# Kernel optimization log

Hardware: AMD Instinct MI355X
Metric: run time of the kernel (lower is better)

Reference implementation:

```python
import jax, jax.numpy as jnp
import numpy as np

N, D, H, E, K = 8192, 1024, 4096, 8, 2


def setup_inputs() -> dict:
    key = jax.random.key(0)
    ks = jax.random.split(key, 4)
    scaled = lambda k, shp, fan: (jax.random.normal(k, shp, jnp.float32) / np.sqrt(fan).astype(np.float32))
    return {
        "x": jax.random.normal(ks[0], (N, D), jnp.float32),
        "Wg": scaled(ks[1], (D, E), D),
        "bg": jnp.zeros((E,), jnp.float32),
        "W1": scaled(ks[2], (E, D, H), D),
        "b1": jnp.zeros((E, H), jnp.float32),
        "W2": scaled(ks[3], (E, H, D), H),
        "b2": jnp.zeros((E, D), jnp.float32),
    }


def reference(x, Wg, bg, W1, b1, W2, b2):
    # Gating: softmax over experts, top-k selection, renormalize top-k probs.
    gate_probs = jax.nn.softmax(x @ Wg + bg, axis=-1)            # [N, E]
    topk_p, topk_i = jax.lax.top_k(gate_probs, K)                # [N, K]
    topk_p = topk_p / topk_p.sum(axis=-1, keepdims=True)
    onehot = jax.nn.one_hot(topk_i, E, dtype=x.dtype)            # [N, K, E]
    # Per-token combine weight for each expert (0 if expert not in top-k).
    w = (onehot * topk_p[..., None]).sum(axis=1)                 # [N, E]

    out = jnp.zeros_like(x)
    for e in range(E):  # fixed small loop over structurally distinct experts
        h = jax.nn.relu(x @ W1[e] + b1[e])                       # dropout = identity (eval)
        out = out + w[:, e:e + 1] * (h @ W2[e] + b2[e])

    # Load-balancing auxiliary loss.
    importance = gate_probs.sum(axis=0)
    importance = importance / importance.sum()
    load = onehot.sum(axis=(0, 1)) / (x.shape[0] * K)            # [E]
    lb_loss = E * (importance * load).sum()
    return out, lb_loss
```

## Files before the change

kernel.cpp:

```cpp
#include <hip/hip_runtime.h>
#include <hip/hip_bf16.h>
#include <math.h>

#define NTOK 8192
#define DDIM 1024
#define HDIM 4096
#define NEXP 8
#define KTOP 2
#define MAXROWS 17408
#define MAXTILES 136

typedef __bf16 bf16x8 __attribute__((ext_vector_type(8)));
typedef float f32x4 __attribute__((ext_vector_type(4)));

#define GAS __attribute__((address_space(1)))
#define LAS __attribute__((address_space(3)))

__device__ __forceinline__ void async16(const void* g, void* l) {
  __builtin_amdgcn_global_load_lds((GAS void*)g, (LAS void*)l, 16, 0, 0);
}

#define XB_OFF     ((size_t)0)
#define W1T_OFF    (XB_OFF + (size_t)NTOK*DDIM*2)
#define ROWOUT_OFF W1T_OFF
#define W2T_OFF    (W1T_OFF + (size_t)NEXP*DDIM*HDIM*2)
#define HB_OFF     (W2T_OFF + (size_t)NEXP*HDIM*DDIM*2)
#define ROWTOK_OFF (HB_OFF + (size_t)MAXROWS*HDIM*2)
#define ROWW_OFF   (ROWTOK_OFF + (size_t)MAXROWS*4)
#define TOKE_OFF   (ROWW_OFF + (size_t)MAXROWS*4)
#define TOKW_OFF   (TOKE_OFF + (size_t)NTOK*KTOP*4)
#define TOKROW_OFF (TOKW_OFF + (size_t)NTOK*KTOP*4)
#define TILEE_OFF  (TOKROW_OFF + (size_t)NTOK*KTOP*4)
#define CNT_OFF    (TILEE_OFF + (size_t)256*4)
#define POS_OFF    (CNT_OFF + 64)
#define IMP_OFF    (POS_OFF + 64)
#define META_OFF   (IMP_OFF + 64)

__global__ void init_kernel(int* counts, float* importance) {
  if (threadIdx.x < NEXP) { counts[threadIdx.x] = 0; importance[threadIdx.x] = 0.f; }
}

__global__ void cast_x_kernel(const float* __restrict__ src, __hip_bfloat16* __restrict__ dst) {
  size_t i = ((size_t)blockIdx.x * blockDim.x + threadIdx.x) * 4;
  if (i < (size_t)NTOK * DDIM) {
    float4 v = *(const float4*)(src + i);
    dst[i + 0] = __float2bfloat16(v.x);
    dst[i + 1] = __float2bfloat16(v.y);
    dst[i + 2] = __float2bfloat16(v.z);
    dst[i + 3] = __float2bfloat16(v.w);
  }
}

__global__ __launch_bounds__(256) void transpose_cast_kernel(
    const float* __restrict__ src, __hip_bfloat16* __restrict__ dst, int R, int C) {
  __shared__ float tile[64][65];
  const int e = blockIdx.z;
  const float* s = src + (size_t)e * R * C;
  __hip_bfloat16* d = dst + (size_t)e * R * C;
  const int c0 = blockIdx.x * 64, r0 = blockIdx.y * 64;
  const int tc = (threadIdx.x & 15) * 4;
  const int tr = threadIdx.x >> 4;
#pragma unroll
  for (int p = 0; p < 4; ++p) {
    float4 v = *(const float4*)&s[(size_t)(r0 + tr + p * 16) * C + c0 + tc];
    tile[tr + p * 16][tc + 0] = v.x;
    tile[tr + p * 16][tc + 1] = v.y;
    tile[tr + p * 16][tc + 2] = v.z;
    tile[tr + p * 16][tc + 3] = v.w;
  }
  __syncthreads();
  const int oc = threadIdx.x >> 4;
  const int orr = (threadIdx.x & 15) * 4;
#pragma unroll
  for (int p = 0; p < 4; ++p) {
    const int c = oc + p * 16;
    __hip_bfloat16 tmp[4];
    tmp[0] = __float2bfloat16(tile[orr + 0][c]);
    tmp[1] = __float2bfloat16(tile[orr + 1][c]);
    tmp[2] = __float2bfloat16(tile[orr + 2][c]);
    tmp[3] = __float2bfloat16(tile[orr + 3][c]);
    *(ushort4*)&d[(size_t)(c0 + c) * R + r0 + orr] = *(ushort4*)tmp;
  }
}

__global__ __launch_bounds__(256) void gating_kernel(
    const float* __restrict__ x, const float* __restrict__ Wg, const float* __restrict__ bg,
    int* __restrict__ tok_e, float* __restrict__ tok_w,
    int* __restrict__ counts, float* __restrict__ importance) {
  const int tid = threadIdx.x, wid = tid >> 6, lane = tid & 63;
  const int t = blockIdx.x * 32 + wid * 8 + (lane >> 3);
  const int e = lane & 7;
  const float* xr = x + (size_t)t * DDIM;
  double dot = 0.0;
  for (int d = 0; d < DDIM; d += 4) {
    float4 xv = *(const float4*)(xr + d);
    dot += (double)xv.x * (double)Wg[(d + 0) * NEXP + e];
    dot += (double)xv.y * (double)Wg[(d + 1) * NEXP + e];
    dot += (double)xv.z * (double)Wg[(d + 2) * NEXP + e];
    dot += (double)xv.w * (double)Wg[(d + 3) * NEXP + e];
  }
  double logit = dot + (double)bg[e];
  double m = logit;
  for (int off = 1; off < 8; off <<= 1) {
    double o = __shfl_xor(m, off, 64);
    m = o > m ? o : m;
  }
  double p = exp(logit - m);
  double s = p;
  for (int off = 1; off < 8; off <<= 1) s += __shfl_xor(s, off, 64);
  float prob = (float)(p / s);

  __shared__ float imp[NEXP];
  __shared__ int cnt[NEXP];
  if (tid < NEXP) { imp[tid] = 0.f; cnt[tid] = 0; }
  __syncthreads();
  atomicAdd(&imp[e], prob);

  float bp = prob; int be = e;
  for (int off = 1; off < 8; off <<= 1) {
    float op = __shfl_xor(bp, off, 64); int oe = __shfl_xor(be, off, 64);
    if (op > bp || (op == bp && oe < be)) { bp = op; be = oe; }
  }
  float p2 = (e == be) ? -1.f : prob;
  float sp = p2; int se = e;
  for (int off = 1; off < 8; off <<= 1) {
    float op = __shfl_xor(sp, off, 64); int oe = __shfl_xor(se, off, 64);
    if (op > sp || (op == sp && oe < se)) { sp = op; se = oe; }
  }
  if (e == 0) {
    float tsum = bp + sp;
    tok_e[t * 2 + 0] = be; tok_e[t * 2 + 1] = se;
    tok_w[t * 2 + 0] = bp / tsum; tok_w[t * 2 + 1] = sp / tsum;
    atomicAdd(&cnt[be], 1); atomicAdd(&cnt[se], 1);
  }
  __syncthreads();
  if (tid < NEXP) {
    atomicAdd(&counts[tid], cnt[tid]);
    atomicAdd(&importance[tid], imp[tid]);
  }
}

__global__ void offsets_kernel(const int* __restrict__ counts, int* pos, int* tile_expert,
                               int* meta, int* row_token) {
  if (threadIdx.x == 0) {
    int pb = 0, tb = 0;
    for (int e = 0; e < NEXP; e++) {
      pos[e] = pb;
      int tiles = (counts[e] + 127) >> 7;
      for (int tt = 0; tt < tiles; ++tt) tile_expert[tb + tt] = e;
      pb += tiles * 128; tb += tiles;
    }
    meta[0] = tb;
  }
  __syncthreads();
  for (int i = threadIdx.x; i < MAXROWS; i += blockDim.x) row_token[i] = -1;
}

__global__ void scatter_kernel(const int* __restrict__ tok_e, const float* __restrict__ tok_w,
                               int* __restrict__ pos, int* __restrict__ row_token,
                               float* __restrict__ row_weight, int* __restrict__ tok_row) {
  __shared__ int lcnt[NEXP], lbase[NEXP];
  const int t = blockIdx.x * 256 + threadIdx.x;
  if (threadIdx.x < NEXP) lcnt[threadIdx.x] = 0;
  __syncthreads();
  const int e0 = tok_e[t * 2 + 0], e1 = tok_e[t * 2 + 1];
  const int s0 = atomicAdd(&lcnt[e0], 1);
  const int s1 = atomicAdd(&lcnt[e1], 1);
  __syncthreads();
  if (threadIdx.x < NEXP) lbase[threadIdx.x] = atomicAdd(&pos[threadIdx.x], lcnt[threadIdx.x]);
  __syncthreads();
  int r0 = lbase[e0] + s0; row_token[r0] = t; row_weight[r0] = tok_w[t * 2 + 0]; tok_row[t * 2 + 0] = r0;
  int r1 = lbase[e1] + s1; row_token[r1] = t; row_weight[r1] = tok_w[t * 2 + 1]; tok_row[t * 2 + 1] = r1;
}

template<int NDIM, int KDIM, int NCOLT, bool GATHER, bool RELU>
__global__ __launch_bounds__(512, 2) void moe_gemm_kernel(
    const __hip_bfloat16* __restrict__ Ag, const __hip_bfloat16* __restrict__ Bg,
    const float* __restrict__ bias, __hip_bfloat16* __restrict__ Cg,
    const int* __restrict__ row_token, const int* __restrict__ tile_expert,
    const int* __restrict__ meta) {
  const int id = blockIdx.x;
  const int v = (id & 7) * ((int)gridDim.x >> 3) + (id >> 3);
  const int ty = v / NCOLT, cx = v % NCOLT;
  if (ty >= meta[0]) return;
  const int e = tile_expert[ty];
  const int r0 = ty * 128;
  const int n0 = cx * 256;
  const int tid = threadIdx.x, wid = tid >> 6, lane = tid & 63;
  const int wm = wid >> 2, wn = wid & 3;
  const int fr = lane & 15;
  const int NT = KDIM / 64;

  __shared__ __align__(16) __hip_bfloat16 Al[2][128][64];
  __shared__ __align__(16) __hip_bfloat16 Bl[2][256][64];

  const int l8 = lane >> 3;
  const int gsrc = (lane & 7) ^ l8;
  const __hip_bfloat16* aptr[2];
  const __hip_bfloat16* bptr0[2];
  const __hip_bfloat16* bptr1[2];
#pragma unroll
  for (int i = 0; i < 2; ++i) {
    const int c = wid * 2 + i;
    const int arow = r0 + c * 8 + l8;
    if (GATHER) {
      int t = row_token[arow]; if (t < 0) t = 0;
      aptr[i] = Ag + (size_t)t * KDIM + gsrc * 8;
    } else {
      aptr[i] = Ag + (size_t)arow * KDIM + gsrc * 8;
    }
    bptr0[i] = Bg + ((size_t)e * NDIM + n0 + c * 8 + l8) * KDIM + gsrc * 8;
    bptr1[i] = bptr0[i] + (size_t)128 * KDIM;
  }

#define ST_A(buf, kk)  do { _Pragma("unroll") for (int i = 0; i < 2; ++i) \
    async16(aptr[i]  + (kk) * 64, &Al[buf][(wid * 2 + i) * 8][0]); } while (0)
#define ST_B0(buf, kk) do { _Pragma("unroll") for (int i = 0; i < 2; ++i) \
    async16(bptr0[i] + (kk) * 64, &Bl[buf][(wid * 2 + i) * 8][0]); } while (0)
#define ST_B1(buf, kk) do { _Pragma("unroll") for (int i = 0; i < 2; ++i) \
    async16(bptr1[i] + (kk) * 64, &Bl[buf][128 + (wid * 2 + i) * 8][0]); } while (0)

  const int g4 = lane >> 4, r7 = lane & 7;
  const int s0e = ((0 + g4) ^ r7) * 8;
  const int s1e = ((4 + g4) ^ r7) * 8;

  f32x4 acc[4][4] = {};

  ST_A(0, 0); ST_B0(0, 0); ST_B1(0, 0);
  ST_A(1, 1); ST_B0(1, 1);
  asm volatile("s_waitcnt vmcnt(6)" ::: "memory");
  __builtin_amdgcn_sched_barrier(0);
  __builtin_amdgcn_s_barrier();

#pragma unroll 1
  for (int kt = 0; kt < NT; ++kt) {
    const int cur = kt & 1, nxt = cur ^ 1;
    const int kk1 = (kt + 1 < NT) ? kt + 1 : NT - 1;
    const int kk2 = (kt + 2 < NT) ? kt + 2 : NT - 1;
    bf16x8 av[4][2], bv[2][2];
#pragma unroll
    for (int mi = 0; mi < 4; ++mi) {
      av[mi][0] = *(const bf16x8*)&Al[cur][wm * 64 + mi * 16 + fr][s0e];
      av[mi][1] = *(const bf16x8*)&Al[cur][wm * 64 + mi * 16 + fr][s1e];
    }
#pragma unroll
    for (int j = 0; j < 2; ++j) {
      bv[j][0] = *(const bf16x8*)&Bl[cur][wn * 32 + j * 16 + fr][s0e];
      bv[j][1] = *(const bf16x8*)&Bl[cur][wn * 32 + j * 16 + fr][s1e];
    }
    ST_B1(nxt, kk1);
    __builtin_amdgcn_s_barrier();
    asm volatile("s_waitcnt lgkmcnt(0)" ::: "memory");
    __builtin_amdgcn_sched_barrier(0);
    __builtin_amdgcn_s_setprio(1);
#pragma unroll
    for (int mi = 0; mi < 4; ++mi)
#pragma unroll
      for (int j = 0; j < 2; ++j)
#pragma unroll
        for (int k = 0; k < 2; ++k)
          acc[mi][j] = __builtin_amdgcn_mfma_f32_16x16x32_bf16(av[mi][k], bv[j][k], acc[mi][j], 0, 0, 0);
    __builtin_amdgcn_s_setprio(0);
    asm volatile("s_waitcnt vmcnt(6)" ::: "memory");
    __builtin_amdgcn_sched_barrier(0);
    __builtin_amdgcn_s_barrier();
#pragma unroll
    for (int j = 0; j < 2; ++j) {
      bv[j][0] = *(const bf16x8*)&Bl[cur][128 + wn * 32 + j * 16 + fr][s0e];
      bv[j][1] = *(const bf16x8*)&Bl[cur][128 + wn * 32 + j * 16 + fr][s1e];
    }
    ST_A(cur, kk2); ST_B0(cur, kk2);
    __builtin_amdgcn_s_barrier();
    asm volatile("s_waitcnt lgkmcnt(0)" ::: "memory");
    __builtin_amdgcn_sched_barrier(0);
    __builtin_amdgcn_s_setprio(1);
#pragma unroll
    for (int mi = 0; mi < 4; ++mi)
#pragma unroll
      for (int j = 0; j < 2; ++j)
#pragma unroll
        for (int k = 0; k < 2; ++k)
          acc[mi][2 + j] = __builtin_amdgcn_mfma_f32_16x16x32_bf16(av[mi][k], bv[j][k], acc[mi][2 + j], 0, 0, 0);
    __builtin_amdgcn_s_setprio(0);
    asm volatile("s_waitcnt vmcnt(6)" ::: "memory");
    __builtin_amdgcn_sched_barrier(0);
    __builtin_amdgcn_s_barrier();
  }
#undef ST_A
#undef ST_B0
#undef ST_B1
  asm volatile("s_waitcnt vmcnt(0)" ::: "memory");

  const int crow = (lane >> 4) * 4;
  const int ccol = lane & 15;
#pragma unroll
  for (int nj = 0; nj < 4; ++nj) {
    const int gc = n0 + (nj >> 1) * 128 + wn * 32 + (nj & 1) * 16 + ccol;
    const float bv_ = bias[e * NDIM + gc];
#pragma unroll
    for (int mi = 0; mi < 4; ++mi) {
      const int grb = r0 + wm * 64 + mi * 16 + crow;
#pragma unroll
      for (int r = 0; r < 4; ++r) {
        float vv = acc[mi][nj][r] + bv_;
        if (RELU) vv = vv > 0.f ? vv : 0.f;
        Cg[(size_t)(grb + r) * NDIM + gc] = __float2bfloat16(vv);
      }
    }
  }
}

__global__ __launch_bounds__(256) void combine_kernel(
    const __hip_bfloat16* __restrict__ rowout, const int* __restrict__ tok_row,
    const float* __restrict__ row_weight, float* __restrict__ out) {
  const int idx = blockIdx.x * 256 + threadIdx.x;
  const int t = idx >> 7;
  const int d = (idx & 127) * 8;
  const int r0 = tok_row[t * 2 + 0], r1 = tok_row[t * 2 + 1];
  const float w0 = row_weight[r0], w1 = row_weight[r1];
  bf16x8 a = *(const bf16x8*)&rowout[(size_t)r0 * DDIM + d];
  bf16x8 b = *(const bf16x8*)&rowout[(size_t)r1 * DDIM + d];
  float o[8];
#pragma unroll
  for (int k = 0; k < 8; k++) o[k] = w0 * (float)a[k] + w1 * (float)b[k];
  float* dst = out + (size_t)t * DDIM + d;
  *(float4*)(dst + 0) = make_float4(o[0], o[1], o[2], o[3]);
  *(float4*)(dst + 4) = make_float4(o[4], o[5], o[6], o[7]);
}

__global__ void finalize_kernel(const float* __restrict__ importance,
                                const int* __restrict__ counts, float* __restrict__ lb_out) {
  if (threadIdx.x == 0 && blockIdx.x == 0) {
    float s = 0.f;
    for (int e = 0; e < NEXP; e++) s += importance[e];
    float lb = 0.f;
    for (int e = 0; e < NEXP; e++)
      lb += (importance[e] / s) * ((float)counts[e] / (float)(NTOK * KTOP));
    lb_out[0] = (float)NEXP * lb;
  }
}

extern "C" void kernel_launch(void* const* d_in, const int* in_sizes, int n_in,
                              void* d_out, int out_size, void* d_ws, size_t ws_size,
                              hipStream_t stream) {
  (void)in_sizes; (void)n_in; (void)out_size; (void)ws_size;
  const float* x  = (const float*)d_in[0];
  const float* Wg = (const float*)d_in[1];
  const float* bg = (const float*)d_in[2];
  const float* W1 = (const float*)d_in[3];
  const float* b1 = (const float*)d_in[4];
  const float* W2 = (const float*)d_in[5];
  const float* b2 = (const float*)d_in[6];
  float* out = (float*)d_out;

  char* ws = (char*)d_ws;
  __hip_bfloat16* xb     = (__hip_bfloat16*)(ws + XB_OFF);
  __hip_bfloat16* w1t    = (__hip_bfloat16*)(ws + W1T_OFF);
  __hip_bfloat16* rowout = (__hip_bfloat16*)(ws + ROWOUT_OFF);
  __hip_bfloat16* w2t    = (__hip_bfloat16*)(ws + W2T_OFF);
  __hip_bfloat16* hb     = (__hip_bfloat16*)(ws + HB_OFF);
  int*   row_token  = (int*)(ws + ROWTOK_OFF);
  float* row_weight = (float*)(ws + ROWW_OFF);
  int*   tok_e   = (int*)(ws + TOKE_OFF);
  float* tok_w   = (float*)(ws + TOKW_OFF);
  int*   tok_row = (int*)(ws + TOKROW_OFF);
  int*   tile_e  = (int*)(ws + TILEE_OFF);
  int*   counts  = (int*)(ws + CNT_OFF);
  int*   pos     = (int*)(ws + POS_OFF);
  float* importance = (float*)(ws + IMP_OFF);
  int*   meta    = (int*)(ws + META_OFF);

  init_kernel<<<1, 64, 0, stream>>>(counts, importance);
  cast_x_kernel<<<NTOK * DDIM / 4 / 256, 256, 0, stream>>>(x, xb);
  transpose_cast_kernel<<<dim3(HDIM / 64, DDIM / 64, NEXP), 256, 0, stream>>>(W1, w1t, DDIM, HDIM);
  transpose_cast_kernel<<<dim3(DDIM / 64, HDIM / 64, NEXP), 256, 0, stream>>>(W2, w2t, HDIM, DDIM);
  gating_kernel<<<NTOK / 32, 256, 0, stream>>>(x, Wg, bg, tok_e, tok_w, counts, importance);
  offsets_kernel<<<1, 256, 0, stream>>>(counts, pos, tile_e, meta, row_token);
  scatter_kernel<<<NTOK / 256, 256, 0, stream>>>(tok_e, tok_w, pos, row_token, row_weight, tok_row);
  moe_gemm_kernel<HDIM, DDIM, HDIM / 256, true, true>
      <<<MAXTILES * (HDIM / 256), 512, 0, stream>>>(xb, w1t, b1, hb, row_token, tile_e, meta);
  moe_gemm_kernel<DDIM, HDIM, DDIM / 256, false, false>
      <<<MAXTILES * (DDIM / 256), 512, 0, stream>>>(hb, w2t, b2, rowout, row_token, tile_e, meta);
  combine_kernel<<<NTOK * 128 / 256, 256, 0, stream>>>(rowout, tok_row, row_weight, out);
  finalize_kernel<<<1, 64, 0, stream>>>(importance, counts, out + (size_t)NTOK * DDIM);
}
```

Before: 839.1 us.

## Enlarge MoE GEMM tiles to 256x256 with triple-buffered BK=32 pipeline

Doubles the row tile from 128 to 256 rows per block, which halves the number of tiles and raises arithmetic intensity per loaded B element. The K step shrinks from 64 to 32, and LDS is reorganised into three stages with a rotating buffer index, replacing the split B0/B1 double-buffer scheme. The XOR swizzle is dropped, so LDS bank conflicts may appear. Each expert now pads up to a multiple of 256 rows, so there is more wasted work per expert, and the 128 fp32 accumulators per lane increase register pressure under launch_bounds(512,2).

```diff
diff --git a/kernel.cpp b/kernel.cpp
--- a/kernel.cpp
+++ b/kernel.cpp
@@ -7,8 +7,8 @@
 #define HDIM 4096
 #define NEXP 8
 #define KTOP 2
-#define MAXROWS 17408
-#define MAXTILES 136
+#define MAXROWS 18432
+#define MAXTILES 72
 
 typedef __bf16 bf16x8 __attribute__((ext_vector_type(8)));
 typedef float f32x4 __attribute__((ext_vector_type(4)));
@@ -146,9 +146,9 @@
     int pb = 0, tb = 0;
     for (int e = 0; e < NEXP; e++) {
       pos[e] = pb;
-      int tiles = (counts[e] + 127) >> 7;
+      int tiles = (counts[e] + 255) >> 8;
       for (int tt = 0; tt < tiles; ++tt) tile_expert[tb + tt] = e;
-      pb += tiles * 128; tb += tiles;
+      pb += tiles * 256; tb += tiles;
     }
     meta[0] = tb;
   }
@@ -184,127 +184,110 @@
   const int ty = v / NCOLT, cx = v % NCOLT;
   if (ty >= meta[0]) return;
   const int e = tile_expert[ty];
-  const int r0 = ty * 128;
+  const int r0 = ty * 256;
   const int n0 = cx * 256;
   const int tid = threadIdx.x, wid = tid >> 6, lane = tid & 63;
   const int wm = wid >> 2, wn = wid & 3;
-  const int fr = lane & 15;
-  const int NT = KDIM / 64;
-
-  __shared__ __align__(16) __hip_bfloat16 Al[2][128][64];
-  __shared__ __align__(16) __hip_bfloat16 Bl[2][256][64];
-
-  const int l8 = lane >> 3;
-  const int gsrc = (lane & 7) ^ l8;
-  const __hip_bfloat16* aptr[2];
-  const __hip_bfloat16* bptr0[2];
-  const __hip_bfloat16* bptr1[2];
-#pragma unroll
-  for (int i = 0; i < 2; ++i) {
-    const int c = wid * 2 + i;
-    const int arow = r0 + c * 8 + l8;
-    if (GATHER) {
-      int t = row_token[arow]; if (t < 0) t = 0;
-      aptr[i] = Ag + (size_t)t * KDIM + gsrc * 8;
-    } else {
-      aptr[i] = Ag + (size_t)arow * KDIM + gsrc * 8;
-    }
-    bptr0[i] = Bg + ((size_t)e * NDIM + n0 + c * 8 + l8) * KDIM + gsrc * 8;
-    bptr1[i] = bptr0[i] + (size_t)128 * KDIM;
-  }
-
-#define ST_A(buf, kk)  do { _Pragma("unroll") for (int i = 0; i < 2; ++i) \
-    async16(aptr[i]  + (kk) * 64, &Al[buf][(wid * 2 + i) * 8][0]); } while (0)
-#define ST_B0(buf, kk) do { _Pragma("unroll") for (int i = 0; i < 2; ++i) \
-    async16(bptr0[i] + (kk) * 64, &Bl[buf][(wid * 2 + i) * 8][0]); } while (0)
-#define ST_B1(buf, kk) do { _Pragma("unroll") for (int i = 0; i < 2; ++i) \
-    async16(bptr1[i] + (kk) * 64, &Bl[buf][128 + (wid * 2 + i) * 8][0]); } while (0)
-
-  const int g4 = lane >> 4, r7 = lane & 7;
-  const int s0e = ((0 + g4) ^ r7) * 8;
-  const int s1e = ((4 + g4) ^ r7) * 8;
-
-  f32x4 acc[4][4] = {};
-
-  ST_A(0, 0); ST_B0(0, 0); ST_B1(0, 0);
-  ST_A(1, 1); ST_B0(1, 1);
-  asm volatile("s_waitcnt vmcnt(6)" ::: "memory");
+  const int fr = lane & 15, g4 = lane >> 4;
+  const int NT = KDIM / 32;
+
+  __shared__ __align__(16) __hip_bfloat16 Al[3][256][32];
+  __shared__ __align__(16) __hip_bfloat16 Bl[3][256][32];
+
+  const int srow0 = (wid * 2 + 0) * 16 + (lane >> 2);
+  const int srow1 = (wid * 2 + 1) * 16 + (lane >> 2);
+  const int sslot = (lane & 3) * 8;
+  const __hip_bfloat16 *ap0, *ap1;
+  if (GATHER) {
+    int t0 = row_token[r0 + srow0]; if (t0 < 0) t0 = 0;
+    int t1 = row_token[r0 + srow1]; if (t1 < 0) t1 = 0;
+    ap0 = Ag + (size_t)t0 * KDIM + sslot;
+    ap1 = Ag + (size_t)t1 * KDIM + sslot;
+  } else {
+    ap0 = Ag + (size_t)(r0 + srow0) * KDIM + sslot;
+    ap1 = Ag + (size_t)(r0 + srow1) * KDIM + sslot;
+  }
+  const __hip_bfloat16* bp0 = Bg + ((size_t)e * NDIM + n0 + srow0) * KDIM + sslot;
+  const __hip_bfloat16* bp1 = Bg + ((size_t)e * NDIM + n0 + srow1) * KDIM + sslot;
+  const int ldsr0 = (wid * 2 + 0) * 16, ldsr1 = (wid * 2 + 1) * 16;
+
+  f32x4 acc[8][4] = {};
+
+  async16(ap0, &Al[0][ldsr0][0]);
+  async16(ap1, &Al[0][ldsr1][0]);
+  async16(bp0, &Bl[0][ldsr0][0]);
+  async16(bp1, &Bl[0][ldsr1][0]);
+  async16(ap0 + 32, &Al[1][ldsr0][0]);
+  async16(ap1 + 32, &Al[1][ldsr1][0]);
+  async16(bp0 + 32, &Bl[1][ldsr0][0]);
+  async16(bp1 + 32, &Bl[1][ldsr1][0]);
+  asm volatile("s_waitcnt vmcnt(4)" ::: "memory");
   __builtin_amdgcn_sched_barrier(0);
   __builtin_amdgcn_s_barrier();
-
+  __builtin_amdgcn_sched_barrier(0);
+
+  int bc = 0, bn = 1, bnn = 2;
 #pragma unroll 1
   for (int kt = 0; kt < NT; ++kt) {
-    const int cur = kt & 1, nxt = cur ^ 1;
-    const int kk1 = (kt + 1 < NT) ? kt + 1 : NT - 1;
-    const int kk2 = (kt + 2 < NT) ? kt + 2 : NT - 1;
-    bf16x8 av[4][2], bv[2][2];
-#pragma unroll
-    for (int mi = 0; mi < 4; ++mi) {
-      av[mi][0] = *(const bf16x8*)&Al[cur][wm * 64 + mi * 16 + fr][s0e];
-      av[mi][1] = *(const bf16x8*)&Al[cur][wm * 64 + mi * 16 + fr][s1e];
-    }
-#pragma unroll
-    for (int j = 0; j < 2; ++j) {
-      bv[j][0] = *(const bf16x8*)&Bl[cur][wn * 32 + j * 16 + fr][s0e];
-      bv[j][1] = *(const bf16x8*)&Bl[cur][wn * 32 + j * 16 + fr][s1e];
-    }
-    ST_B1(nxt, kk1);
+    const int kk = (kt + 2 < NT) ? kt + 2 : NT - 1;
+    bf16x8 a0[4], a1[4], bv[4];
+#pragma unroll
+    for (int i = 0; i < 4; ++i)
+      a0[i] = *(const bf16x8*)&Al[bc][wm * 128 + i * 16 + fr][g4 * 8];
+#pragma unroll
+    for (int j = 0; j < 4; ++j)
+      bv[j] = *(const bf16x8*)&Bl[bc][wn * 64 + j * 16 + fr][g4 * 8];
+    async16(ap0 + (size_t)kk * 32, &Al[bnn][ldsr0][0]);
+    async16(ap1 + (size_t)kk * 32, &Al[bnn][ldsr1][0]);
+    async16(bp0 + (size_t)kk * 32, &Bl[bnn][ldsr0][0]);
+    async16(bp1 + (size_t)kk * 32, &Bl[bnn][ldsr1][0]);
     __builtin_amdgcn_s_barrier();
     asm volatile("s_waitcnt lgkmcnt(0)" ::: "memory");
     __builtin_amdgcn_sched_barrier(0);
     __builtin_amdgcn_s_setprio(1);
 #pragma unroll
-    for (int mi = 0; mi < 4; ++mi)
-#pragma unroll
-      for (int j = 0; j < 2; ++j)
-#pragma unroll
-        for (int k = 0; k < 2; ++k)
-          acc[mi][j] = __builtin_amdgcn_mfma_f32_16x16x32_bf16(av[mi][k], bv[j][k], acc[mi][j], 0, 0, 0);
+    for (int i = 0; i < 4; ++i)
+#pragma unroll
+      for (int j = 0; j < 4; ++j)
+        acc[i][j] = __builtin_amdgcn_mfma_f32_16x16x32_bf16(a0[i], bv[j], acc[i][j], 0, 0, 0);
     __builtin_amdgcn_s_setprio(0);
-    asm volatile("s_waitcnt vmcnt(6)" ::: "memory");
-    __builtin_amdgcn_sched_barrier(0);
     __builtin_amdgcn_s_barrier();
-#pragma unroll
-    for (int j = 0; j < 2; ++j) {
-      bv[j][0] = *(const bf16x8*)&Bl[cur][128 + wn * 32 + j * 16 + fr][s0e];
-      bv[j][1] = *(const bf16x8*)&Bl[cur][128 + wn * 32 + j * 16 + fr][s1e];
-    }
-    ST_A(cur, kk2); ST_B0(cur, kk2);
+    __builtin_amdgcn_sched_barrier(0);
+#pragma unroll
+    for (int i = 0; i < 4; ++i)
+      a1[i] = *(const bf16x8*)&Al[bc][wm * 128 + 64 + i * 16 + fr][g4 * 8];
     __builtin_amdgcn_s_barrier();
     asm volatile("s_waitcnt lgkmcnt(0)" ::: "memory");
     __builtin_amdgcn_sched_barrier(0);
     __builtin_amdgcn_s_setprio(1);
 #pragma unroll
-    for (int mi = 0; mi < 4; ++mi)
-#pragma unroll
-      for (int j = 0; j < 2; ++j)
-#pragma unroll
-        for (int k = 0; k < 2; ++k)
-          acc[mi][2 + j] = __builtin_amdgcn_mfma_f32_16x16x32_bf16(av[mi][k], bv[j][k], acc[mi][2 + j], 0, 0, 0);
+    for (int i = 0; i < 4; ++i)
+#pragma unroll
+      for (int j = 0; j < 4; ++j)
+        acc[4 + i][j] = __builtin_amdgcn_mfma_f32_16x16x32_bf16(a1[i], bv[j], acc[4 + i][j], 0, 0, 0);
     __builtin_amdgcn_s_setprio(0);
-    asm volatile("s_waitcnt vmcnt(6)" ::: "memory");
+    asm volatile("s_waitcnt vmcnt(4)" ::: "memory");
     __builtin_amdgcn_sched_barrier(0);
     __builtin_amdgcn_s_barrier();
-  }
-#undef ST_A
-#undef ST_B0
-#undef ST_B1
+    __builtin_amdgcn_sched_barrier(0);
+    const int tmp = bc; bc = bn; bn = bnn; bnn = tmp;
+  }
   asm volatile("s_waitcnt vmcnt(0)" ::: "memory");
 
   const int crow = (lane >> 4) * 4;
   const int ccol = lane & 15;
 #pragma unroll
-  for (int nj = 0; nj < 4; ++nj) {
-    const int gc = n0 + (nj >> 1) * 128 + wn * 32 + (nj & 1) * 16 + ccol;
-    const float bv_ = bias[e * NDIM + gc];
-#pragma unroll
-    for (int mi = 0; mi < 4; ++mi) {
-      const int grb = r0 + wm * 64 + mi * 16 + crow;
+  for (int j = 0; j < 4; ++j) {
+    const int gc = n0 + wn * 64 + j * 16 + ccol;
+    const float bb = bias[e * NDIM + gc];
+#pragma unroll
+    for (int m = 0; m < 8; ++m) {
+      const int gr = r0 + wm * 128 + m * 16 + crow;
 #pragma unroll
       for (int r = 0; r < 4; ++r) {
-        float vv = acc[mi][nj][r] + bv_;
+        float vv = acc[m][j][r] + bb;
         if (RELU) vv = vv > 0.f ? vv : 0.f;
-        Cg[(size_t)(grb + r) * NDIM + gc] = __float2bfloat16(vv);
+        Cg[(size_t)(gr + r) * NDIM + gc] = __float2bfloat16(vv);
       }
     }
   }
```

Result: slower. 936.9 us (+11.6%).
